# Performance work log

Measured on AMD Instinct MI355X. Metric: run time of the kernel, lower is better.

## Reference

```python
import jax, jax.numpy as jnp
import numpy as np

N_NODES = 100_000
N_EDGES_RAND = 800_000
N_GRAPHS = 2048
IN_FEATS = 74        # CanonicalAtomFeaturizer size
HEADS = 4            # dgllife GAT default num_heads
OUT_FEATS = 32       # dgllife GAT default hidden_feats=[32,32]
PRED_DIM = 128
NEG_SLOPE = 0.2      # dgllife default alpha


def setup_inputs() -> dict:
    key = jax.random.key(0)
    ks = jax.random.split(key, 16)
    feats = jax.random.normal(ks[0], (N_NODES, IN_FEATS), jnp.float32)
    src_r = jax.random.randint(ks[1], (N_EDGES_RAND,), 0, N_NODES, dtype=jnp.int32)
    dst_r = jax.random.randint(ks[2], (N_EDGES_RAND,), 0, N_NODES, dtype=jnp.int32)
    loops = jnp.arange(N_NODES, dtype=jnp.int32)  # self-loops -> no zero in-degree
    src = jnp.concatenate([src_r, loops])
    dst = jnp.concatenate([dst_r, loops])
    # sorted, every graph non-empty, ~49 nodes per molecule
    graph_ids = ((jnp.arange(N_NODES, dtype=jnp.int64) * N_GRAPHS) // N_NODES).astype(jnp.int32)

    def lin(k, i, o):
        return (jax.random.normal(k, (i, o), jnp.float32) / np.sqrt(i)).astype(jnp.float32)

    HF = HEADS * OUT_FEATS
    return {
        'feats': feats, 'src': src, 'dst': dst, 'graph_ids': graph_ids,
        'fc1_w': lin(ks[3], IN_FEATS, HF),
        'attn_l1': jax.random.normal(ks[4], (HEADS, OUT_FEATS), jnp.float32) * 0.1,
        'attn_r1': jax.random.normal(ks[5], (HEADS, OUT_FEATS), jnp.float32) * 0.1,
        'res1_w': lin(ks[6], IN_FEATS, HF),   # residual proj (in != heads*out)
        'bias1': jnp.zeros((HF,), jnp.float32),
        'fc2_w': lin(ks[7], HF, HF),
        'attn_l2': jax.random.normal(ks[8], (HEADS, OUT_FEATS), jnp.float32) * 0.1,
        'attn_r2': jax.random.normal(ks[9], (HEADS, OUT_FEATS), jnp.float32) * 0.1,
        'bias2': jnp.zeros((HF,), jnp.float32),
        'ww': lin(ks[10], OUT_FEATS, 1),
        'wb': jnp.zeros((1,), jnp.float32),
        'tw': lin(ks[11], 2 * OUT_FEATS, PRED_DIM),
        'tb': jnp.zeros((PRED_DIM,), jnp.float32),
    }


def _gat_conv(h, src, dst, fc_w, attn_l, attn_r, bias, res):
    # h: (N, Din) -> (N, H, F). Faithful to dgl.nn.GATConv (bias=True, residual=True).
    N = h.shape[0]
    feat = (h @ fc_w).reshape(N, HEADS, OUT_FEATS)          # (N,H,F)
    el = jnp.sum(feat * attn_l, axis=-1)                    # (N,H)
    er = jnp.sum(feat * attn_r, axis=-1)                    # (N,H)
    e = jax.nn.leaky_relu(el[src] + er[dst], NEG_SLOPE)     # (E,H)
    # edge softmax over incoming edges of each dst node (numerically stable)
    emax = jax.ops.segment_max(e, dst, num_segments=N)      # (N,H)
    ee = jnp.exp(e - emax[dst])
    denom = jax.ops.segment_sum(ee, dst, num_segments=N)    # (N,H)
    a = ee / denom[dst]                                     # (E,H)
    rst = jax.ops.segment_sum(a[:, :, None] * feat[src], dst, num_segments=N)  # (N,H,F)
    return rst + res + bias.reshape(1, HEADS, OUT_FEATS)


def reference(feats, src, dst, graph_ids, fc1_w, attn_l1, attn_r1, res1_w, bias1,
              fc2_w, attn_l2, attn_r2, bias2, ww, wb, tw, tb):
    N = feats.shape[0]
    # Layer 1: residual needs projection (74 != 128); agg 'flatten' + ELU
    res1 = (feats @ res1_w).reshape(N, HEADS, OUT_FEATS)
    h1 = _gat_conv(feats, src, dst, fc1_w, attn_l1, attn_r1, bias1, res1)
    h1 = jax.nn.elu(h1.reshape(N, HEADS * OUT_FEATS))
    # Layer 2: identity residual (128 == heads*out); agg 'mean', no activation
    res2 = h1.reshape(N, HEADS, OUT_FEATS)
    h2 = _gat_conv(h1, src, dst, fc2_w, attn_l2, attn_r2, bias2, res2)
    node_feats = jnp.mean(h2, axis=1)                       # (N, 32)
    # WeightedSumAndMax readout
    w = jax.nn.sigmoid(node_feats @ ww + wb)                # (N,1)
    h_sum = jax.ops.segment_sum(w * node_feats, graph_ids, num_segments=N_GRAPHS)
    h_max = jax.ops.segment_max(node_feats, graph_ids, num_segments=N_GRAPHS)
    g = jnp.concatenate([h_sum, h_max], axis=-1)            # (B, 64)
    return g @ tw + tb                                      # (B, PRED_DIM)
```

## Files before the change

### kernel.cpp

```cpp
#include <hip/hip_runtime.h>
#include <hip/hip_bf16.h>


#define HEADS 4
#define OUTF 32
#define HF 128
#define IN_FEATS 74
#define PRED_DIM 128
#define NEG_SLOPE 0.2f
#define NEG_INF_ENC 0x007fffffu
#define LOG2E 1.4426950408889634f
#define KP1 48
#define KP2 64
#define LSTR1 52
#define LSTR2 68

typedef __hip_bfloat16 bf16;
typedef __hip_bfloat162 bf16x2;
typedef __attribute__((ext_vector_type(8))) short bf16x8v;
typedef __attribute__((ext_vector_type(4))) float f32x4v;
typedef __attribute__((ext_vector_type(2))) float f32x2v;

__device__ __forceinline__ unsigned enc_f(float f) {
  unsigned u = __float_as_uint(f);
  return (u & 0x80000000u) ? ~u : (u | 0x80000000u);
}
__device__ __forceinline__ float dec_f(unsigned k) {
  return (k & 0x80000000u) ? __uint_as_float(k & 0x7fffffffu)
                           : __uint_as_float(~k);
}
__device__ __forceinline__ unsigned pack_bf16(float a, float b) {
  bf16x2 h = __float22bfloat162_rn(make_float2(a, b));
  return *(unsigned*)&h;
}
__device__ __forceinline__ float2 unpack_bf16(unsigned u) {
  bf16x2 h = *(bf16x2*)&u;
  return __bfloat1622float2(h);
}
__device__ __forceinline__ float lrelu(float v) {
  return fmaxf(v, NEG_SLOPE * v);
}

__global__ __launch_bounds__(256) void hist_prep(
    const int* __restrict__ dst, int* __restrict__ deg,
    int* __restrict__ rank, float* __restrict__ hsum,
    unsigned* __restrict__ hmax, int E, int g32,
    const float* __restrict__ W1, const float* __restrict__ W2,
    const float* __restrict__ W3, unsigned* __restrict__ WT1,
    unsigned* __restrict__ WT2, unsigned* __restrict__ WT3) {
  int t = blockIdx.x * 256 + threadIdx.x;
  if (t < g32) {
    hsum[t] = 0.f;
    hmax[t] = NEG_INF_ENC;
  }
  if (t < 128 * KP1) {
    int c = t / KP1, kp = t % KP1;
    int k = kp * 2;
    float a1 = (k < IN_FEATS) ? W1[k * HF + c] : 0.f;
    float b1 = (k + 1 < IN_FEATS) ? W1[(k + 1) * HF + c] : 0.f;
    float a2 = (k < IN_FEATS) ? W2[k * HF + c] : 0.f;
    float b2 = (k + 1 < IN_FEATS) ? W2[(k + 1) * HF + c] : 0.f;
    WT1[t] = pack_bf16(a1, b1);
    WT2[t] = pack_bf16(a2, b2);
  } else if (t - 128 * KP1 < 128 * KP2) {
    int u = t - 128 * KP1;
    int c = u / KP2, kp = u % KP2;
    int k = kp * 2;
    WT3[u] = pack_bf16(W3[k * HF + c], W3[(k + 1) * HF + c]);
  }
  if (t < E) rank[t] = atomicAdd(&deg[dst[t]], 1);
}

__global__ __launch_bounds__(256) void scan12_kernel(
    const int* __restrict__ deg, int* __restrict__ row_ptr,
    int* __restrict__ bsum, int* __restrict__ bpre,
    int* __restrict__ ticket, int N, int E) {
  const int base = blockIdx.x * 2048;
  const int tbase = base + threadIdx.x * 8;
  int vals[8];
  int tsum = 0;
#pragma unroll
  for (int i = 0; i < 8; ++i) {
    int idx = tbase + i;
    vals[i] = (idx < N) ? deg[idx] : 0;
    tsum += vals[i];
  }
  const int lane = threadIdx.x & 63, wv = threadIdx.x >> 6;
  int incl = tsum;
#pragma unroll
  for (int off = 1; off < 64; off <<= 1) {
    int nv = __shfl_up(incl, off);
    if (lane >= off) incl += nv;
  }
  __shared__ int wsum[4];
  __shared__ int isLast;
  if (lane == 63) wsum[wv] = incl;
  __syncthreads();
  int woff = 0;
  for (int w = 0; w < wv; ++w) woff += wsum[w];
  int run = woff + incl - tsum;
#pragma unroll
  for (int i = 0; i < 8; ++i) {
    int idx = tbase + i;
    if (idx < N) row_ptr[idx] = run;
    run += vals[i];
  }
  if (threadIdx.x == 255) {
    bsum[blockIdx.x] = woff + incl;
    __threadfence();
    int t = atomicAdd(ticket, 1);
    isLast = (t == (int)gridDim.x - 1);
  }
  __syncthreads();
  if (isLast) {
    if (threadIdx.x < 64) {
      __threadfence();
      const int NB = gridDim.x;
      int running = 0;
      for (int c = 0; c < NB; c += 64) {
        int v = (c + lane < NB) ? bsum[c + lane] : 0;
        int incl2 = v;
#pragma unroll
        for (int off = 1; off < 64; off <<= 1) {
          int nv = __shfl_up(incl2, off);
          if (lane >= off) incl2 += nv;
        }
        if (c + lane < NB) bpre[c + lane] = running + incl2 - v;
        running += __shfl(incl2, 63);
      }
    }
    __syncthreads();
    if (threadIdx.x == 0) row_ptr[N] = E - bpre[N >> 11];
  }
}


template <int K>
__device__ __forceinline__ bf16x8v load_a_f32(const float* __restrict__ X,
                                              int row, int N, int ks, int q) {
  unsigned v[4] = {0u, 0u, 0u, 0u};
  if (row < N) {
    const float* base = X + (size_t)row * K;
    int k = ks * 32 + q * 8;
#pragma unroll
    for (int j = 0; j < 4; ++j) {
      int kk = k + j * 2;
      if (kk + 1 < K) {
        float2 f = *(const float2*)&base[kk];
        v[j] = pack_bf16(f.x, f.y);
      } else if (kk < K) {
        v[j] = pack_bf16(base[kk], 0.f);
      }
    }
  }
  union { unsigned u[4]; bf16x8v v8; } r;
  r.u[0] = v[0]; r.u[1] = v[1]; r.u[2] = v[2]; r.u[3] = v[3];
  return r.v8;
}

template <int KP, int LSTR, int THREADS>
__device__ __forceinline__ void stage_w(const unsigned* __restrict__ WT,
                                        unsigned* wl, int tid) {
#pragma unroll
  for (int u = tid; u < 128 * (KP / 4); u += THREADS) {
    int row = u / (KP / 4), c4 = u % (KP / 4);
    uint4 v = *(const uint4*)&WT[row * KP + c4 * 4];
    *(uint4*)&wl[row * LSTR + c4 * 4] = v;
  }
}

__device__ __forceinline__ void scores_epilogue(
    const f32x4v* acc, const float* __restrict__ attn_l,
    const float* __restrict__ attn_r, float* __restrict__ el,
    float* __restrict__ er, int n0, int w, int q, int cc, int N) {
#pragma unroll
  for (int r = 0; r < 4; ++r) {
    int n = n0 + w * 16 + q * 4 + r;
    float pls[4], prs[4];
#pragma unroll
    for (int h = 0; h < 4; ++h) {
      float pl = acc[2 * h][r] * attn_l[h * 32 + cc] +
                 acc[2 * h + 1][r] * attn_l[h * 32 + 16 + cc];
      float pr = acc[2 * h][r] * attn_r[h * 32 + cc] +
                 acc[2 * h + 1][r] * attn_r[h * 32 + 16 + cc];
#pragma unroll
      for (int off = 1; off < 16; off <<= 1) {
        pl += __shfl_xor(pl, off);
        pr += __shfl_xor(pr, off);
      }
      pls[h] = pl;
      prs[h] = pr;
    }
    if (cc == 0 && n < N) {
#pragma unroll
      for (int h = 0; h < 4; ++h) {
        el[n * HEADS + h] = pls[h] * LOG2E;
        er[n * HEADS + h] = prs[h] * LOG2E;
      }
    }
  }
}

__global__ __launch_bounds__(512) void scat_mfma1(
    const int* __restrict__ src, const int* __restrict__ dst,
    const int* __restrict__ row_ptr, const int* __restrict__ bpre,
    const int* __restrict__ rank, int* __restrict__ ssorted, int E, int gblk,
    const float* __restrict__ X, const unsigned* __restrict__ WT1,
    const unsigned* __restrict__ WT2, const float* __restrict__ attn_l,
    const float* __restrict__ attn_r, bf16* __restrict__ outA,
    bf16* __restrict__ outB, float* __restrict__ el, float* __restrict__ er,
    int N) {
  __shared__ __align__(16) unsigned wlds[2][128 * LSTR1];
  if ((int)blockIdx.x >= gblk) {
    int e = ((int)blockIdx.x - gblk) * 512 + threadIdx.x;
    if (e >= E) return;
    if (e < 16) ssorted[E + e] = 0;
    int d = dst[e];
    ssorted[row_ptr[d] + bpre[d >> 11] + rank[e]] = src[e];
    return;
  }
  const int tid = threadIdx.x;
  stage_w<KP1, LSTR1, 512>(WT1, &wlds[0][0], tid);
  stage_w<KP1, LSTR1, 512>(WT2, &wlds[1][0], tid);
  __syncthreads();

  const int w = tid >> 6;
  const int lane = tid & 63;
  const int cc = lane & 15;
  const int q = lane >> 4;
  const int n0 = blockIdx.x * 128;
  const int arow = n0 + w * 16 + cc;

  f32x4v acc1[8], acc2[8];
#pragma unroll
  for (int t = 0; t < 8; ++t) {
    acc1[t] = f32x4v{0.f, 0.f, 0.f, 0.f};
    acc2[t] = f32x4v{0.f, 0.f, 0.f, 0.f};
  }

  constexpr int KSTEPS = (IN_FEATS + 31) / 32;
#pragma unroll
  for (int ks = 0; ks < KSTEPS; ++ks) {
    bf16x8v a = load_a_f32<IN_FEATS>(X, arow, N, ks, q);
#pragma unroll
    for (int t = 0; t < 8; ++t) {
      bf16x8v b1 =
          *(const bf16x8v*)&wlds[0][(t * 16 + cc) * LSTR1 + ks * 16 + q * 4];
      bf16x8v b2 =
          *(const bf16x8v*)&wlds[1][(t * 16 + cc) * LSTR1 + ks * 16 + q * 4];
      acc1[t] = __builtin_amdgcn_mfma_f32_16x16x32_bf16(a, b1, acc1[t], 0, 0, 0);
      acc2[t] = __builtin_amdgcn_mfma_f32_16x16x32_bf16(a, b2, acc2[t], 0, 0, 0);
    }
  }
#pragma unroll
  for (int r = 0; r < 4; ++r) {
    int n = n0 + w * 16 + q * 4 + r;
    if (n < N) {
#pragma unroll
      for (int t = 0; t < 8; ++t) {
        outA[(size_t)n * HF + t * 16 + cc] = __float2bfloat16(acc1[t][r]);
        outB[(size_t)n * HF + t * 16 + cc] = __float2bfloat16(acc2[t][r]);
      }
    }
  }
  scores_epilogue(acc1, attn_l, attn_r, el, er, n0, w, q, cc, N);
}

template <int K, int KP, int LSTR>
__global__ __launch_bounds__(512) void mfma_gemm(
    const bf16* __restrict__ X, const unsigned* __restrict__ WT,
    const float* __restrict__ attn_l, const float* __restrict__ attn_r,
    bf16* __restrict__ out, float* __restrict__ el, float* __restrict__ er,
    int N) {
  __shared__ __align__(16) unsigned wlds[128 * LSTR];
  const int tid = threadIdx.x;
  stage_w<KP, LSTR, 512>(WT, wlds, tid);
  __syncthreads();

  const int w = tid >> 6;
  const int lane = tid & 63;
  const int cc = lane & 15;
  const int q = lane >> 4;
  const int n0 = blockIdx.x * 128;
  const int arow = n0 + w * 16 + cc;

  f32x4v acc[8];
#pragma unroll
  for (int t = 0; t < 8; ++t) acc[t] = f32x4v{0.f, 0.f, 0.f, 0.f};

  constexpr int KSTEPS = (K + 31) / 32;
#pragma unroll
  for (int ks = 0; ks < KSTEPS; ++ks) {
    bf16x8v a = *(const bf16x8v*)&X[(size_t)arow * K + ks * 32 + q * 8];
#pragma unroll
    for (int t = 0; t < 8; ++t) {
      bf16x8v b =
          *(const bf16x8v*)&wlds[(t * 16 + cc) * LSTR + ks * 16 + q * 4];
      acc[t] = __builtin_amdgcn_mfma_f32_16x16x32_bf16(a, b, acc[t], 0, 0, 0);
    }
  }
#pragma unroll
  for (int r = 0; r < 4; ++r) {
    int n = n0 + w * 16 + q * 4 + r;
    if (n < N) {
#pragma unroll
      for (int t = 0; t < 8; ++t)
        out[(size_t)n * HF + t * 16 + cc] = __float2bfloat16(acc[t][r]);
    }
  }
  scores_epilogue(acc, attn_l, attn_r, el, er, n0, w, q, cc, N);
}


#define E8_LOAD(i, e_)                                                      \
  const int s##i = __builtin_amdgcn_readfirstlane(ssorted[e_]);             \
  const float xl##i = el[(unsigned)s##i * HEADS + h];                       \
  const unsigned fu##i = *(const unsigned*)&feat[(unsigned)s##i * HF + c2];
#define E8_CALC(i)                                                          \
  {                                                                         \
    float xx = __builtin_amdgcn_exp2f(lrelu(xl##i + ern));                  \
    f32x2v ff;                                                              \
    ff.x = __uint_as_float(fu##i << 16);                                    \
    ff.y = __uint_as_float(fu##i & 0xffff0000u);                            \
    ssum += xx;                                                             \
    axy = __builtin_elementwise_fma(f32x2v{xx, xx}, ff, axy);               \
  }
#define E8_CALC_PRED(i, e_)                                                 \
  {                                                                         \
    float xx = __builtin_amdgcn_exp2f(lrelu(xl##i + ern));                  \
    xx = ((e_) + i < re) ? xx : 0.f;                                        \
    f32x2v ff;                                                              \
    ff.x = __uint_as_float(fu##i << 16);                                    \
    ff.y = __uint_as_float(fu##i & 0xffff0000u);                            \
    ssum += xx;                                                             \
    axy = __builtin_elementwise_fma(f32x2v{xx, xx}, ff, axy);               \
  }

#define AGG_LOOP                                                            \
  f32x2v axy = {0.f, 0.f};                                                  \
  float ssum = 0.f;                                                         \
  const int dg = re - rb;                                                   \
  if (dg <= 8) {                                                            \
    E8_LOAD(0, rb) E8_LOAD(1, rb + 1) E8_LOAD(2, rb + 2)                    \
    E8_LOAD(3, rb + 3) E8_LOAD(4, rb + 4) E8_LOAD(5, rb + 5)                \
    E8_LOAD(6, rb + 6) E8_LOAD(7, rb + 7)                                   \
    E8_CALC_PRED(0, rb) E8_CALC_PRED(1, rb) E8_CALC_PRED(2, rb)             \
    E8_CALC_PRED(3, rb) E8_CALC_PRED(4, rb) E8_CALC_PRED(5, rb)             \
    E8_CALC_PRED(6, rb) E8_CALC_PRED(7, rb)                                 \
  } else if (dg <= 16) {                                                    \
    E8_LOAD(0, rb) E8_LOAD(1, rb + 1) E8_LOAD(2, rb + 2)                    \
    E8_LOAD(3, rb + 3) E8_LOAD(4, rb + 4) E8_LOAD(5, rb + 5)                \
    E8_LOAD(6, rb + 6) E8_LOAD(7, rb + 7)                                   \
    E8_LOAD(8, rb + 8) E8_LOAD(9, rb + 9) E8_LOAD(10, rb + 10)              \
    E8_LOAD(11, rb + 11) E8_LOAD(12, rb + 12) E8_LOAD(13, rb + 13)          \
    E8_LOAD(14, rb + 14) E8_LOAD(15, rb + 15)                               \
    E8_CALC(0) E8_CALC(1) E8_CALC(2) E8_CALC(3)                             \
    E8_CALC(4) E8_CALC(5) E8_CALC(6) E8_CALC(7)                             \
    E8_CALC_PRED(8, rb) E8_CALC_PRED(9, rb) E8_CALC_PRED(10, rb)            \
    E8_CALC_PRED(11, rb) E8_CALC_PRED(12, rb) E8_CALC_PRED(13, rb)          \
    E8_CALC_PRED(14, rb) E8_CALC_PRED(15, rb)                               \
  } else {                                                                  \
    int e = rb;                                                             \
    for (; e + 8 <= re; e += 8) {                                           \
      E8_LOAD(0, e) E8_LOAD(1, e + 1) E8_LOAD(2, e + 2) E8_LOAD(3, e + 3)   \
      E8_LOAD(4, e + 4) E8_LOAD(5, e + 5) E8_LOAD(6, e + 6)                 \
      E8_LOAD(7, e + 7)                                                     \
      E8_CALC(0) E8_CALC(1) E8_CALC(2) E8_CALC(3)                           \
      E8_CALC(4) E8_CALC(5) E8_CALC(6) E8_CALC(7)                           \
    }                                                                       \
    if (e < re) {                                                           \
      E8_LOAD(0, e) E8_LOAD(1, e + 1) E8_LOAD(2, e + 2) E8_LOAD(3, e + 3)   \
      E8_LOAD(4, e + 4) E8_LOAD(5, e + 5) E8_LOAD(6, e + 6)                 \
      E8_LOAD(7, e + 7)                                                     \
      E8_CALC_PRED(0, e) E8_CALC_PRED(1, e) E8_CALC_PRED(2, e)              \
      E8_CALC_PRED(3, e) E8_CALC_PRED(4, e) E8_CALC_PRED(5, e)              \
      E8_CALC_PRED(6, e) E8_CALC_PRED(7, e)                                 \
    }                                                                       \
  }                                                                         \
  float ax = axy.x, ay = axy.y;

__global__ __launch_bounds__(256) void agg1_fused(
    const int* __restrict__ row_ptr, const int* __restrict__ bpre,
    const int* __restrict__ ssorted, const float* __restrict__ el,
    const float* __restrict__ er, const bf16* __restrict__ feat,
    const bf16* __restrict__ res, bf16* __restrict__ H,
    const float* __restrict__ bias, int N) {
  int n = blockIdx.x * 4 + (threadIdx.x >> 6);
  if (n >= N) return;
  const int lane = threadIdx.x & 63;
  const int c2 = lane * 2, h = lane >> 4;
  const int rb =
      __builtin_amdgcn_readfirstlane(row_ptr[n] + bpre[n >> 11]);
  const int re =
      __builtin_amdgcn_readfirstlane(row_ptr[n + 1] + bpre[(n + 1) >> 11]);
  const float ern = er[(unsigned)n * HEADS + h];

  AGG_LOOP

  float inv = 1.f / ssum;
  float2 r = unpack_bf16(*(const unsigned*)&res[(unsigned)n * HF + c2]);
  float2 bi = *(const float2*)&bias[c2];
  float vx = fmaf(ax, inv, r.x + bi.x);
  float vy = fmaf(ay, inv, r.y + bi.y);
  vx = (vx > 0.f) ? vx : expm1f(vx);
  vy = (vy > 0.f) ? vy : expm1f(vy);
  *(unsigned*)&H[(unsigned)n * HF + c2] = pack_bf16(vx, vy);
}

__global__ __launch_bounds__(256) void agg2_fused(
    const int* __restrict__ row_ptr, const int* __restrict__ bpre,
    const int* __restrict__ ssorted, const float* __restrict__ el,
    const float* __restrict__ er, const bf16* __restrict__ feat,
    const bf16* __restrict__ h1, const float* __restrict__ bias,
    const float* __restrict__ ww, const float* __restrict__ wb,
    const int* __restrict__ gids, float* __restrict__ hsum,
    unsigned* __restrict__ hmax, int N) {
  int n = blockIdx.x * 4 + (threadIdx.x >> 6);
  if (n >= N) return;
  const int lane = threadIdx.x & 63;
  const int c2 = lane * 2, h = lane >> 4;
  const int rb =
      __builtin_amdgcn_readfirstlane(row_ptr[n] + bpre[n >> 11]);
  const int re =
      __builtin_amdgcn_readfirstlane(row_ptr[n + 1] + bpre[(n + 1) >> 11]);
  const float ern = er[(unsigned)n * HEADS + h];

  AGG_LOOP

  float inv = 1.f / ssum;
  float2 r = unpack_bf16(*(const unsigned*)&h1[(unsigned)n * HF + c2]);
  float2 bi = *(const float2*)&bias[c2];
  ax = fmaf(ax, inv, r.x + bi.x);
  ay = fmaf(ay, inv, r.y + bi.y);
#pragma unroll
  for (int off = 16; off < 64; off <<= 1) {
    ax += __shfl_xor(ax, off);
    ay += __shfl_xor(ay, off);
  }
  ax *= 0.25f;
  ay *= 0.25f;
  int c = c2 & 31;
  float d = fmaf(ax, ww[c], ay * ww[c + 1]);
#pragma unroll
  for (int off = 1; off < 16; off <<= 1) d += __shfl_xor(d, off);
  float wv = 1.f / (1.f + __expf(-(d + wb[0])));
  if (lane < 16) {
    int g = gids[n];
    atomicAdd(&hsum[g * OUTF + c], wv * ax);
    atomicAdd(&hsum[g * OUTF + c + 1], wv * ay);
    atomicMax(&hmax[g * OUTF + c], enc_f(ax));
    atomicMax(&hmax[g * OUTF + c + 1], enc_f(ay));
  }
}

__global__ __launch_bounds__(256) void final_gemm_kernel(
    const float* __restrict__ hsum, const unsigned* __restrict__ hmax,
    const float* __restrict__ tw, const float* __restrict__ tb,
    float* __restrict__ out, int G) {
  __shared__ float tws[64 * PRED_DIM];
  for (int i = threadIdx.x; i < 64 * PRED_DIM; i += 256) tws[i] = tw[i];
  __syncthreads();
  int g = blockIdx.x * 2 + (threadIdx.x >> 7);
  int p = threadIdx.x & 127;
  if (g >= G) return;
  float acc = tb[p];
#pragma unroll
  for (int k = 0; k < OUTF; ++k)
    acc = fmaf(hsum[g * OUTF + k], tws[k * PRED_DIM + p], acc);
#pragma unroll
  for (int k = 0; k < OUTF; ++k)
    acc = fmaf(dec_f(hmax[g * OUTF + k]), tws[(OUTF + k) * PRED_DIM + p], acc);
  out[(size_t)g * PRED_DIM + p] = acc;
}

static inline int cdiv(long long a, int b) { return (int)((a + b - 1) / b); }

extern "C" void kernel_launch(void* const* d_in, const int* in_sizes, int n_in,
                              void* d_out, int out_size, void* d_ws,
                              size_t ws_size, hipStream_t stream) {
  const float* feats   = (const float*)d_in[0];
  const int*   src     = (const int*)d_in[1];
  const int*   dst     = (const int*)d_in[2];
  const int*   gids    = (const int*)d_in[3];
  const float* fc1_w   = (const float*)d_in[4];
  const float* attn_l1 = (const float*)d_in[5];
  const float* attn_r1 = (const float*)d_in[6];
  const float* res1_w  = (const float*)d_in[7];
  const float* bias1   = (const float*)d_in[8];
  const float* fc2_w   = (const float*)d_in[9];
  const float* attn_l2 = (const float*)d_in[10];
  const float* attn_r2 = (const float*)d_in[11];
  const float* bias2   = (const float*)d_in[12];
  const float* ww      = (const float*)d_in[13];
  const float* wb      = (const float*)d_in[14];
  const float* tw      = (const float*)d_in[15];
  const float* tb      = (const float*)d_in[16];
  float* out = (float*)d_out;

  const int N = in_sizes[0] / IN_FEATS;
  const int E = in_sizes[1];
  const int G = out_size / PRED_DIM;
  const int NB = cdiv(N, 2048);

  bf16* A = (bf16*)d_ws;
  bf16* B = A + (size_t)N * HF;
  bf16* H = B + (size_t)N * HF;
  float* el = (float*)(H + (size_t)N * HF);
  float* er = el + (size_t)N * HEADS;
  float* hsum = er + (size_t)N * HEADS;
  unsigned* hmax = (unsigned*)(hsum + (size_t)G * OUTF);
  int* deg     = (int*)(hmax + (size_t)G * OUTF);
  int* ticket  = deg + N;
  int* row_ptr = deg + N + 1;
  int* ssorted = row_ptr + (N + 1);
  int* rank    = ssorted + E + 16;
  int* bsum    = rank + E;
  int* bpre    = bsum + NB;
  unsigned* WT1 = (unsigned*)(((uintptr_t)(bpre + NB) + 15) &
                              ~(uintptr_t)15);
  unsigned* WT2 = WT1 + 128 * KP1;
  unsigned* WT3 = WT2 + 128 * KP1;

  const int gblk = cdiv(N, 128);
  const int nwblk = cdiv(N, 4);
  const int SB = cdiv(E, 256);
  const int SB512 = cdiv(E, 512);

  hipMemsetAsync(deg, 0, (size_t)(N + 1) * sizeof(int), stream);
  hist_prep<<<SB, 256, 0, stream>>>(dst, deg, rank, hsum, hmax, E, G * OUTF,
                                    fc1_w, res1_w, fc2_w, WT1, WT2, WT3);
  scan12_kernel<<<NB, 256, 0, stream>>>(deg, row_ptr, bsum, bpre, ticket, N,
                                        E);

  scat_mfma1<<<gblk + SB512, 512, 0, stream>>>(
      src, dst, row_ptr, bpre, rank, ssorted, E, gblk, feats, WT1, WT2,
      attn_l1, attn_r1, A, B, el, er, N);
  agg1_fused<<<nwblk, 256, 0, stream>>>(row_ptr, bpre, ssorted, el, er, A, B,
                                        H, bias1, N);

  mfma_gemm<HF, KP2, LSTR2><<<gblk, 512, 0, stream>>>(
      H, WT3, attn_l2, attn_r2, A, el, er, N);
  agg2_fused<<<nwblk, 256, 0, stream>>>(row_ptr, bpre, ssorted, el, er, A, H,
                                        bias2, ww, wb, gids, hsum, hmax, N);

  final_gemm_kernel<<<cdiv(G, 2), 256, 0, stream>>>(hsum, hmax, tw, tb, out, G);
}
```

Measured before the change: 311.6 us.

## Store layer-1 features head-major and split layer-1 aggregation per head

Measured after the change: 397.8 us. 27.7% more time.

```diff
diff --git a/kernel.cpp b/kernel.cpp
--- a/kernel.cpp
+++ b/kernel.cpp
@@ -258,8 +258,9 @@
     if (n < N) {
 #pragma unroll
       for (int t = 0; t < 8; ++t) {
-        outA[(size_t)n * HF + t * 16 + cc] = __float2bfloat16(acc1[t][r]);
-        outB[(size_t)n * HF + t * 16 + cc] = __float2bfloat16(acc2[t][r]);
+        size_t off = ((size_t)(t >> 1) * N + n) * 32 + (t & 1) * 16 + cc;
+        outA[off] = __float2bfloat16(acc1[t][r]);
+        outB[off] = __float2bfloat16(acc2[t][r]);
       }
     }
   }
@@ -291,7 +292,7 @@
   constexpr int KSTEPS = (K + 31) / 32;
 #pragma unroll
   for (int ks = 0; ks < KSTEPS; ++ks) {
-    bf16x8v a = *(const bf16x8v*)&X[(size_t)arow * K + ks * 32 + q * 8];
+    bf16x8v a = *(const bf16x8v*)&X[((size_t)ks * N + arow) * 32 + q * 8];
 #pragma unroll
     for (int t = 0; t < 8; ++t) {
       bf16x8v b =
@@ -309,6 +310,79 @@
     }
   }
   scores_epilogue(acc, attn_l, attn_r, el, er, n0, w, q, cc, N);
+}
+
+
+#define H4_LOAD(j, e_)                                                      \
+  const int s##j = ssorted[(e_) + g];                                       \
+  const float xl##j = el[(unsigned)s##j * HEADS + hh];                      \
+  const unsigned fu##j = *(const unsigned*)&fb[(size_t)s##j * 32 + i2];
+#define H4_CALC(j, e_)                                                      \
+  {                                                                         \
+    float xx = __builtin_amdgcn_exp2f(lrelu(xl##j + ern));                  \
+    xx = ((e_) + g < re) ? xx : 0.f;                                        \
+    f32x2v ff;                                                              \
+    ff.x = __uint_as_float(fu##j << 16);                                    \
+    ff.y = __uint_as_float(fu##j & 0xffff0000u);                            \
+    ssum += xx;                                                             \
+    axy = __builtin_elementwise_fma(f32x2v{xx, xx}, ff, axy);               \
+  }
+
+__global__ __launch_bounds__(256) void agg1_fused(
+    const int* __restrict__ row_ptr, const int* __restrict__ bpre,
+    const int* __restrict__ ssorted, const float* __restrict__ el,
+    const float* __restrict__ er, const bf16* __restrict__ featH,
+    const bf16* __restrict__ resH, bf16* __restrict__ H,
+    const float* __restrict__ bias, int N) {
+  int n = blockIdx.x * 4 + (threadIdx.x >> 6);
+  if (n >= N) return;
+  const int hh = blockIdx.y;
+  const int lane = threadIdx.x & 63;
+  const int g = lane >> 4;
+  const int i2 = (lane & 15) * 2;
+  const int rb =
+      __builtin_amdgcn_readfirstlane(row_ptr[n] + bpre[n >> 11]);
+  const int re =
+      __builtin_amdgcn_readfirstlane(row_ptr[n + 1] + bpre[(n + 1) >> 11]);
+  const float ern = er[(unsigned)n * HEADS + hh];
+  const bf16* fb = featH + (size_t)hh * N * 32;
+
+  f32x2v axy = {0.f, 0.f};
+  float ssum = 0.f;
+  const int dg = re - rb;
+  if (dg <= 16) {
+    H4_LOAD(0, rb) H4_LOAD(1, rb + 4) H4_LOAD(2, rb + 8) H4_LOAD(3, rb + 12)
+    H4_CALC(0, rb) H4_CALC(1, rb + 4) H4_CALC(2, rb + 8) H4_CALC(3, rb + 12)
+  } else {
+    int e = rb;
+    for (; e + 16 <= re; e += 16) {
+      H4_LOAD(0, e) H4_LOAD(1, e + 4) H4_LOAD(2, e + 8) H4_LOAD(3, e + 12)
+      H4_CALC(0, e) H4_CALC(1, e + 4) H4_CALC(2, e + 8) H4_CALC(3, e + 12)
+    }
+    if (e < re) {
+      H4_LOAD(0, e) H4_LOAD(1, e + 4) H4_LOAD(2, e + 8) H4_LOAD(3, e + 12)
+      H4_CALC(0, e) H4_CALC(1, e + 4) H4_CALC(2, e + 8) H4_CALC(3, e + 12)
+    }
+  }
+  ssum += __shfl_xor(ssum, 16);
+  ssum += __shfl_xor(ssum, 32);
+  float ax = axy.x, ay = axy.y;
+  ax += __shfl_xor(ax, 16);
+  ax += __shfl_xor(ax, 32);
+  ay += __shfl_xor(ay, 16);
+  ay += __shfl_xor(ay, 32);
+
+  if (lane < 16) {
+    float inv = 1.f / ssum;
+    float2 r = unpack_bf16(
+        *(const unsigned*)&resH[((size_t)hh * N + n) * 32 + i2]);
+    float2 bi = *(const float2*)&bias[hh * 32 + i2];
+    float vx = fmaf(ax, inv, r.x + bi.x);
+    float vy = fmaf(ay, inv, r.y + bi.y);
+    vx = (vx > 0.f) ? vx : expm1f(vx);
+    vy = (vy > 0.f) ? vy : expm1f(vy);
+    *(unsigned*)&H[((size_t)hh * N + n) * 32 + i2] = pack_bf16(vx, vy);
+  }
 }
 
 
@@ -379,34 +453,6 @@
   }                                                                         \
   float ax = axy.x, ay = axy.y;
 
-__global__ __launch_bounds__(256) void agg1_fused(
-    const int* __restrict__ row_ptr, const int* __restrict__ bpre,
-    const int* __restrict__ ssorted, const float* __restrict__ el,
-    const float* __restrict__ er, const bf16* __restrict__ feat,
-    const bf16* __restrict__ res, bf16* __restrict__ H,
-    const float* __restrict__ bias, int N) {
-  int n = blockIdx.x * 4 + (threadIdx.x >> 6);
-  if (n >= N) return;
-  const int lane = threadIdx.x & 63;
-  const int c2 = lane * 2, h = lane >> 4;
-  const int rb =
-      __builtin_amdgcn_readfirstlane(row_ptr[n] + bpre[n >> 11]);
-  const int re =
-      __builtin_amdgcn_readfirstlane(row_ptr[n + 1] + bpre[(n + 1) >> 11]);
-  const float ern = er[(unsigned)n * HEADS + h];
-
-  AGG_LOOP
-
-  float inv = 1.f / ssum;
-  float2 r = unpack_bf16(*(const unsigned*)&res[(unsigned)n * HF + c2]);
-  float2 bi = *(const float2*)&bias[c2];
-  float vx = fmaf(ax, inv, r.x + bi.x);
-  float vy = fmaf(ay, inv, r.y + bi.y);
-  vx = (vx > 0.f) ? vx : expm1f(vx);
-  vy = (vy > 0.f) ? vy : expm1f(vy);
-  *(unsigned*)&H[(unsigned)n * HF + c2] = pack_bf16(vx, vy);
-}
-
 __global__ __launch_bounds__(256) void agg2_fused(
     const int* __restrict__ row_ptr, const int* __restrict__ bpre,
     const int* __restrict__ ssorted, const float* __restrict__ el,
@@ -428,7 +474,8 @@
   AGG_LOOP
 
   float inv = 1.f / ssum;
-  float2 r = unpack_bf16(*(const unsigned*)&h1[(unsigned)n * HF + c2]);
+  float2 r = unpack_bf16(
+      *(const unsigned*)&h1[((size_t)h * N + n) * 32 + (lane & 15) * 2]);
   float2 bi = *(const float2*)&bias[c2];
   ax = fmaf(ax, inv, r.x + bi.x);
   ay = fmaf(ay, inv, r.y + bi.y);
@@ -535,8 +582,8 @@
   scat_mfma1<<<gblk + SB512, 512, 0, stream>>>(
       src, dst, row_ptr, bpre, rank, ssorted, E, gblk, feats, WT1, WT2,
       attn_l1, attn_r1, A, B, el, er, N);
-  agg1_fused<<<nwblk, 256, 0, stream>>>(row_ptr, bpre, ssorted, el, er, A, B,
-                                        H, bias1, N);
+  agg1_fused<<<dim3(nwblk, 4), 256, 0, stream>>>(row_ptr, bpre, ssorted, el,
+                                                 er, A, B, H, bias1, N);
 
   mfma_gemm<HF, KP2, LSTR2><<<gblk, 512, 0, stream>>>(
       H, WT3, attn_l2, attn_r2, A, el, er, N);
```
